# Performance work log

Hardware: AMD Instinct MI355X
Metric: run time of the kernel (lower is better)

Reference implementation:

```python
import jax, jax.numpy as jnp
import numpy as np

KERNEL_MUL = 2.0
KERNEL_NUM = 5


def _mmd_loss(source, target):
    n_s = source.shape[0]
    n_samples = n_s + target.shape[0]
    total = jnp.concatenate([source, target], axis=0)  # [2N, d]
    # Pairwise squared L2 distances via ||a||^2 + ||b||^2 - 2 a.b (same math,
    # avoids materializing the [2N, 2N, d] expanded diff the torch code builds).
    sq = jnp.sum(total * total, axis=1)  # [2N]
    L2 = sq[:, None] + sq[None, :] - 2.0 * (total @ total.T)  # [2N, 2N]
    # torch uses L2_distance.data for bandwidth -> stop_gradient
    bandwidth = jax.lax.stop_gradient(jnp.sum(L2)) / (n_samples ** 2 - n_samples)
    bandwidth = bandwidth / (KERNEL_MUL ** (KERNEL_NUM // 2))
    kernels = sum(jnp.exp(-L2 / (bandwidth * KERNEL_MUL ** i)) for i in range(KERNEL_NUM))
    XX = jnp.mean(kernels[:n_s, :n_s])
    YY = jnp.mean(kernels[n_s:, n_s:])
    XY = jnp.mean(kernels[:n_s, n_s:])
    YX = jnp.mean(kernels[n_s:, :n_s])
    return XX + YY - XY - YX


def setup_inputs() -> dict:
    key = jax.random.key(0)
    k1, k2 = jax.random.split(key)
    source = jax.random.normal(k1, (4096, 64), dtype=jnp.float32)
    target = jax.random.normal(k2, (4096, 64), dtype=jnp.float32)
    return {"source": source, "target": target}


def reference(source, target):
    return _mmd_loss(source, target)
```

## Files before the change

### kernel.cpp

```cpp
#include <hip/hip_runtime.h>
#include <math.h>

#define N_HALF 4096
#define D 64
#define M_TOT 8192
#define NPAIR 2080

typedef _Float16 half8 __attribute__((ext_vector_type(8)));
typedef float f32x4 __attribute__((ext_vector_type(4)));

__device__ _Float16 Fh[M_TOT * D];
__device__ float g_norms[M_TOT];
__device__ float g_pssq[256];
__device__ float g_pcol[256 * D];
__device__ float g_coef;
__device__ double g_part[NPAIR];

__global__ __launch_bounds__(256) void mmd_prep(const float* __restrict__ src,
                                                const float* __restrict__ tgt) {
    __shared__ float cs[D];
    __shared__ float hn[4][16];
    int t = threadIdx.x;
    if (t < D) cs[t] = 0.f;
    __syncthreads();
    int tid = blockIdx.x * 256 + t;
    int l = tid & 63;
    int rs = tid >> 6;
    int s = rs & 1, rt = rs >> 1;
    int row = rt * 16 + (l & 15);
    int k0 = s * 32 + (l >> 4) * 8;
    const float* X = (row < N_HALF) ? src + (size_t)row * D
                                    : tgt + (size_t)(row - N_HALF) * D;
    float4 v0 = ((const float4*)(X + k0))[0];
    float4 v1 = ((const float4*)(X + k0))[1];
    float vs[8] = {v0.x, v0.y, v0.z, v0.w, v1.x, v1.y, v1.z, v1.w};
    half8 h;
    float p = 0.f;
#pragma unroll
    for (int e = 0; e < 8; ++e) {
        h[e] = (_Float16)vs[e];
        p += vs[e] * vs[e];
    }
    ((half8*)Fh)[tid] = h;
#pragma unroll
    for (int e = 0; e < 8; ++e) atomicAdd(&cs[k0 + e], vs[e]);
    p += __shfl_down(p, 32, 64);
    p += __shfl_down(p, 16, 64);
    int w = t >> 6;
    if (l < 16) hn[w][l] = p;
    __syncthreads();
    if (t < 64) {
        float nr = 0.f;
        int tile = t >> 4, r = t & 15;
        if (t < 32) {
            nr = hn[tile * 2][r] + hn[tile * 2 + 1][r];
            g_norms[(blockIdx.x * 2 + tile) * 16 + r] = nr;
        }
        nr += __shfl_down(nr, 32, 64);
        nr += __shfl_down(nr, 16, 64);
        nr += __shfl_down(nr, 8, 64);
        nr += __shfl_down(nr, 4, 64);
        nr += __shfl_down(nr, 2, 64);
        nr += __shfl_down(nr, 1, 64);
        if (t == 0) g_pssq[blockIdx.x] = nr;
    }
    if (t < D) g_pcol[blockIdx.x * D + t] = cs[t];
}

__global__ __launch_bounds__(256) void mmd_bw() {
    __shared__ float scol[4][64];
    __shared__ float sssq[4];
    int t = threadIdx.x, w = t >> 6, l = t & 63;
    float csum = 0.f;
#pragma unroll 16
    for (int q = 0; q < 64; ++q) csum += g_pcol[(w * 64 + q) * 64 + l];
    float sq = g_pssq[w * 64 + l];
#pragma unroll
    for (int off = 32; off; off >>= 1) sq += __shfl_xor(sq, off, 64);
    scol[w][l] = csum;
    if (l == 0) sssq[w] = sq;
    __syncthreads();
    if (t < 64) {
        float colsum = (scol[0][l] + scol[1][l]) + (scol[2][l] + scol[3][l]);
        float s2 = colsum * colsum;
#pragma unroll
        for (int off = 32; off; off >>= 1) s2 += __shfl_xor(s2, off, 64);
        if (t == 0) {
            float ssq = (sssq[0] + sssq[1]) + (sssq[2] + sssq[3]);
            const float M = (float)M_TOT;
            float sumL2 = 2.f * M * ssq - 2.f * s2;
            float bwq = sumL2 / (M * M - M) * 0.25f;
            g_coef = -1.4426950408889634f / (bwq * 16.f);
        }
    }
}

static __device__ inline void decode_pair(int id, int& bi, int& bj) {
    bi = (int)(64.5f - sqrtf(4160.25f - 2.0f * (float)id));
    while ((64 * (bi + 1) - ((bi + 1) * bi) / 2) <= id) ++bi;
    while ((64 * bi - (bi * (bi - 1)) / 2) > id) --bi;
    bj = bi + (id - (64 * bi - (bi * (bi - 1)) / 2));
}

__global__ __launch_bounds__(512) void mmd_main() {
    __shared__ float sred[8];
    int t = threadIdx.x, w = t >> 6, l = t & 63;
    int wr = w >> 2, wc = w & 3;
    float g0 = g_coef;
    float c2 = -2.f * g0;
    const half8* FH = (const half8*)Fh;

    int bi, bj;
    decode_pair(blockIdx.x, bi, bj);

    float nas[4][4];
#pragma unroll
    for (int m = 0; m < 4; ++m) {
        float4 v = *(const float4*)&g_norms[bi * 128 + wr * 64 + m * 16 + (l >> 4) * 4];
        nas[m][0] = v.x * g0; nas[m][1] = v.y * g0;
        nas[m][2] = v.z * g0; nas[m][3] = v.w * g0;
    }
    float nbv[2];
#pragma unroll
    for (int n = 0; n < 2; ++n)
        nbv[n] = g_norms[bj * 128 + wc * 32 + n * 16 + (l & 15)] * g0;

    f32x4 acc[4][2] = {};
#pragma unroll
    for (int s = 0; s < 2; ++s) {
        half8 bh[2];
#pragma unroll
        for (int n = 0; n < 2; ++n)
            bh[n] = FH[((bj * 8 + wc * 2 + n) * 2 + s) * 64 + l];
#pragma unroll
        for (int m = 0; m < 4; ++m) {
            half8 ah = FH[((bi * 8 + wr * 4 + m) * 2 + s) * 64 + l];
#pragma unroll
            for (int n = 0; n < 2; ++n)
                acc[m][n] = __builtin_amdgcn_mfma_f32_16x16x32_f16(ah, bh[n], acc[m][n], 0, 0, 0);
        }
    }

    float part4[4] = {0.f, 0.f, 0.f, 0.f};
#pragma unroll
    for (int m = 0; m < 4; ++m)
#pragma unroll
        for (int n = 0; n < 2; ++n)
#pragma unroll
            for (int r = 0; r < 4; ++r) {
                float t0 = fmaf(acc[m][n][r], c2, nas[m][r] + nbv[n]);
                float k4 = __builtin_amdgcn_exp2f(t0);
                float k3 = k4 * k4;
                float k2 = k3 * k3;
                float k1 = k2 * k2;
                float k0 = k1 * k1;
                part4[r] += (k4 + k3) + ((k2 + k1) + k0);
            }
    float part = (part4[0] + part4[1]) + (part4[2] + part4[3]);

#pragma unroll
    for (int off = 32; off; off >>= 1) part += __shfl_down(part, off, 64);
    if (l == 0) sred[w] = part;
    __syncthreads();
    if (t == 0) {
        float tot = ((sred[0] + sred[1]) + (sred[2] + sred[3])) +
                    ((sred[4] + sred[5]) + (sred[6] + sred[7]));
        float sgn = ((bi < 32) == (bj < 32)) ? 1.f : -1.f;
        float scl = (bi == bj) ? 1.f : 2.f;
        g_part[blockIdx.x] = (double)tot * (double)(sgn * scl);
    }
}

__global__ __launch_bounds__(256) void mmd_out(float* __restrict__ out) {
    __shared__ double wred[4];
    int t = threadIdx.x;
    double s = 0.0;
    for (int i = t; i < NPAIR; i += 256) s += g_part[i];
#pragma unroll
    for (int off = 32; off; off >>= 1) s += __shfl_down(s, off, 64);
    if ((t & 63) == 0) wred[t >> 6] = s;
    __syncthreads();
    if (t == 0)
        out[0] = (float)((wred[0] + wred[1] + wred[2] + wred[3]) * (1.0 / 16777216.0));
}

extern "C" void kernel_launch(void* const* d_in, const int* in_sizes, int n_in,
                              void* d_out, int out_size, void* d_ws, size_t ws_size,
                              hipStream_t stream) {
    const float* src = (const float*)d_in[0];
    const float* tgt = (const float*)d_in[1];
    float* out = (float*)d_out;

    mmd_prep<<<256, 256, 0, stream>>>(src, tgt);
    mmd_bw<<<1, 256, 0, stream>>>();
    mmd_main<<<NPAIR, 512, 0, stream>>>();
    mmd_out<<<1, 256, 0, stream>>>(out);
}
```

Baseline: 35.13 us.

## Fuse bandwidth reduction into main kernel and process two tile pairs per block

Removes the single-block bandwidth kernel launch. Every main block now recomputes the bandwidth coefficient from the per-block column sums and squared-norm partials. Each block also handles two tile pairs instead of one, halving the grid and the number of partial results. This trades a kernel launch and a serialized tiny kernel for redundant reads of about 64KB of partials in every block, with fewer blocks to absorb that overhead.

```diff
diff --git a/kernel.cpp b/kernel.cpp
--- a/kernel.cpp
+++ b/kernel.cpp
@@ -5,6 +5,7 @@
 #define D 64
 #define M_TOT 8192
 #define NPAIR 2080
+#define NBLK 1040
 
 typedef _Float16 half8 __attribute__((ext_vector_type(8)));
 typedef float f32x4 __attribute__((ext_vector_type(4)));
@@ -13,8 +14,7 @@
 __device__ float g_norms[M_TOT];
 __device__ float g_pssq[256];
 __device__ float g_pcol[256 * D];
-__device__ float g_coef;
-__device__ double g_part[NPAIR];
+__device__ double g_part[NBLK];
 
 __global__ __launch_bounds__(256) void mmd_prep(const float* __restrict__ src,
                                                 const float* __restrict__ tgt) {
@@ -67,34 +67,6 @@
     if (t < D) g_pcol[blockIdx.x * D + t] = cs[t];
 }
 
-__global__ __launch_bounds__(256) void mmd_bw() {
-    __shared__ float scol[4][64];
-    __shared__ float sssq[4];
-    int t = threadIdx.x, w = t >> 6, l = t & 63;
-    float csum = 0.f;
-#pragma unroll 16
-    for (int q = 0; q < 64; ++q) csum += g_pcol[(w * 64 + q) * 64 + l];
-    float sq = g_pssq[w * 64 + l];
-#pragma unroll
-    for (int off = 32; off; off >>= 1) sq += __shfl_xor(sq, off, 64);
-    scol[w][l] = csum;
-    if (l == 0) sssq[w] = sq;
-    __syncthreads();
-    if (t < 64) {
-        float colsum = (scol[0][l] + scol[1][l]) + (scol[2][l] + scol[3][l]);
-        float s2 = colsum * colsum;
-#pragma unroll
-        for (int off = 32; off; off >>= 1) s2 += __shfl_xor(s2, off, 64);
-        if (t == 0) {
-            float ssq = (sssq[0] + sssq[1]) + (sssq[2] + sssq[3]);
-            const float M = (float)M_TOT;
-            float sumL2 = 2.f * M * ssq - 2.f * s2;
-            float bwq = sumL2 / (M * M - M) * 0.25f;
-            g_coef = -1.4426950408889634f / (bwq * 16.f);
-        }
-    }
-}
-
 static __device__ inline void decode_pair(int id, int& bi, int& bj) {
     bi = (int)(64.5f - sqrtf(4160.25f - 2.0f * (float)id));
     while ((64 * (bi + 1) - ((bi + 1) * bi) / 2) <= id) ++bi;
@@ -103,71 +75,103 @@
 }
 
 __global__ __launch_bounds__(512) void mmd_main() {
+    __shared__ float scol[8][64];
+    __shared__ float sssq[8];
     __shared__ float sred[8];
     int t = threadIdx.x, w = t >> 6, l = t & 63;
     int wr = w >> 2, wc = w & 3;
-    float g0 = g_coef;
-    float c2 = -2.f * g0;
     const half8* FH = (const half8*)Fh;
 
-    int bi, bj;
-    decode_pair(blockIdx.x, bi, bj);
-
-    float nas[4][4];
-#pragma unroll
-    for (int m = 0; m < 4; ++m) {
-        float4 v = *(const float4*)&g_norms[bi * 128 + wr * 64 + m * 16 + (l >> 4) * 4];
-        nas[m][0] = v.x * g0; nas[m][1] = v.y * g0;
-        nas[m][2] = v.z * g0; nas[m][3] = v.w * g0;
-    }
-    float nbv[2];
-#pragma unroll
-    for (int n = 0; n < 2; ++n)
-        nbv[n] = g_norms[bj * 128 + wc * 32 + n * 16 + (l & 15)] * g0;
-
-    f32x4 acc[4][2] = {};
-#pragma unroll
-    for (int s = 0; s < 2; ++s) {
-        half8 bh[2];
+    {
+        float csum = 0.f;
+#pragma unroll 8
+        for (int q = 0; q < 32; ++q) csum += g_pcol[((w * 32 + q) << 6) + l];
+        float sq = (l < 32) ? g_pssq[w * 32 + l] : 0.f;
+#pragma unroll
+        for (int off = 32; off; off >>= 1) sq += __shfl_xor(sq, off, 64);
+        scol[w][l] = csum;
+        if (l == 0) sssq[w] = sq;
+    }
+    __syncthreads();
+    float g0, c2;
+    {
+        float colsum = ((scol[0][l] + scol[1][l]) + (scol[2][l] + scol[3][l])) +
+                       ((scol[4][l] + scol[5][l]) + (scol[6][l] + scol[7][l]));
+        float s2 = colsum * colsum;
+#pragma unroll
+        for (int off = 32; off; off >>= 1) s2 += __shfl_xor(s2, off, 64);
+        float ssq = ((sssq[0] + sssq[1]) + (sssq[2] + sssq[3])) +
+                    ((sssq[4] + sssq[5]) + (sssq[6] + sssq[7]));
+        const float M = (float)M_TOT;
+        float sumL2 = 2.f * M * ssq - 2.f * s2;
+        float bwq = sumL2 / (M * M - M) * 0.25f;
+        g0 = -1.4426950408889634f / (bwq * 16.f);
+        c2 = -2.f * g0;
+    }
+
+    float mypart = 0.f;
+#pragma unroll
+    for (int p = 0; p < 2; ++p) {
+        int id = blockIdx.x * 2 + p;
+        int bi, bj;
+        decode_pair(id, bi, bj);
+
+        float nas[4][4];
+#pragma unroll
+        for (int m = 0; m < 4; ++m) {
+            float4 v = *(const float4*)&g_norms[bi * 128 + wr * 64 + m * 16 + (l >> 4) * 4];
+            nas[m][0] = v.x; nas[m][1] = v.y; nas[m][2] = v.z; nas[m][3] = v.w;
+        }
+        float nbv[2];
 #pragma unroll
         for (int n = 0; n < 2; ++n)
-            bh[n] = FH[((bj * 8 + wc * 2 + n) * 2 + s) * 64 + l];
-#pragma unroll
-        for (int m = 0; m < 4; ++m) {
-            half8 ah = FH[((bi * 8 + wr * 4 + m) * 2 + s) * 64 + l];
+            nbv[n] = g_norms[bj * 128 + wc * 32 + n * 16 + (l & 15)];
+
+        f32x4 acc[4][2] = {};
+#pragma unroll
+        for (int s = 0; s < 2; ++s) {
+            half8 bh[2];
 #pragma unroll
             for (int n = 0; n < 2; ++n)
-                acc[m][n] = __builtin_amdgcn_mfma_f32_16x16x32_f16(ah, bh[n], acc[m][n], 0, 0, 0);
+                bh[n] = FH[((bj * 8 + wc * 2 + n) * 2 + s) * 64 + l];
+#pragma unroll
+            for (int m = 0; m < 4; ++m) {
+                half8 ah = FH[((bi * 8 + wr * 4 + m) * 2 + s) * 64 + l];
+#pragma unroll
+                for (int n = 0; n < 2; ++n)
+                    acc[m][n] = __builtin_amdgcn_mfma_f32_16x16x32_f16(ah, bh[n], acc[m][n], 0, 0, 0);
+            }
         }
-    }
-
-    float part4[4] = {0.f, 0.f, 0.f, 0.f};
-#pragma unroll
-    for (int m = 0; m < 4; ++m)
-#pragma unroll
-        for (int n = 0; n < 2; ++n)
-#pragma unroll
-            for (int r = 0; r < 4; ++r) {
-                float t0 = fmaf(acc[m][n][r], c2, nas[m][r] + nbv[n]);
-                float k4 = __builtin_amdgcn_exp2f(t0);
-                float k3 = k4 * k4;
-                float k2 = k3 * k3;
-                float k1 = k2 * k2;
-                float k0 = k1 * k1;
-                part4[r] += (k4 + k3) + ((k2 + k1) + k0);
-            }
-    float part = (part4[0] + part4[1]) + (part4[2] + part4[3]);
-
-#pragma unroll
-    for (int off = 32; off; off >>= 1) part += __shfl_down(part, off, 64);
-    if (l == 0) sred[w] = part;
+
+        float part4[4] = {0.f, 0.f, 0.f, 0.f};
+#pragma unroll
+        for (int m = 0; m < 4; ++m)
+#pragma unroll
+            for (int n = 0; n < 2; ++n)
+#pragma unroll
+                for (int r = 0; r < 4; ++r) {
+                    float t0 = fmaf(acc[m][n][r], c2, (nas[m][r] + nbv[n]) * g0);
+                    float k4 = __builtin_amdgcn_exp2f(t0);
+                    float k3 = k4 * k4;
+                    float k2 = k3 * k3;
+                    float k1 = k2 * k2;
+                    float k0 = k1 * k1;
+                    part4[r] += (k4 + k3) + ((k2 + k1) + k0);
+                }
+        float part = (part4[0] + part4[1]) + (part4[2] + part4[3]);
+        float sgn = ((bi < 32) == (bj < 32)) ? 1.f : -1.f;
+        float scl = (bi == bj) ? 1.f : 2.f;
+        mypart = fmaf(part, sgn * scl, mypart);
+    }
+
+#pragma unroll
+    for (int off = 32; off; off >>= 1) mypart += __shfl_down(mypart, off, 64);
+    if (l == 0) sred[w] = mypart;
     __syncthreads();
     if (t == 0) {
         float tot = ((sred[0] + sred[1]) + (sred[2] + sred[3])) +
                     ((sred[4] + sred[5]) + (sred[6] + sred[7]));
-        float sgn = ((bi < 32) == (bj < 32)) ? 1.f : -1.f;
-        float scl = (bi == bj) ? 1.f : 2.f;
-        g_part[blockIdx.x] = (double)tot * (double)(sgn * scl);
+        g_part[blockIdx.x] = (double)tot;
     }
 }
 
@@ -175,7 +179,7 @@
     __shared__ double wred[4];
     int t = threadIdx.x;
     double s = 0.0;
-    for (int i = t; i < NPAIR; i += 256) s += g_part[i];
+    for (int i = t; i < NBLK; i += 256) s += g_part[i];
 #pragma unroll
     for (int off = 32; off; off >>= 1) s += __shfl_down(s, off, 64);
     if ((t & 63) == 0) wred[t >> 6] = s;
@@ -192,7 +196,6 @@
     float* out = (float*)d_out;
 
     mmd_prep<<<256, 256, 0, stream>>>(src, tgt);
-    mmd_bw<<<1, 256, 0, stream>>>();
-    mmd_main<<<NPAIR, 512, 0, stream>>>();
+    mmd_main<<<NBLK, 512, 0, stream>>>();
     mmd_out<<<1, 256, 0, stream>>>(out);
 }
```

Result: slower. 36.43 us (+3.7%).
